# Optimization experiments

Measured on AMD Instinct MI355X. Metric: run time of the kernel, lower is better.

## Reference

```python
import jax, jax.numpy as jnp
import numpy as np
from math import factorial

MAXL = 5
TAUS = [8, 8, 8, 8, 8, 8]
OUT_TAUS = [8, 8, 8, 8, 8, 8]
BM_EPS = 1e-5
BATCH = 1024


def _cg_coeff(l1, l2, l, m1, m2, m):
    # Standard Clebsch-Gordan coefficient <l1 m1 l2 m2 | l m> (Racah formula).
    if m1 + m2 != m:
        return 0.0
    f = factorial
    pre = ((2 * l + 1) * f(l + l1 - l2) * f(l - l1 + l2) * f(l1 + l2 - l) / f(l1 + l2 + l + 1)) ** 0.5
    pre *= (f(l + m) * f(l - m) * f(l1 - m1) * f(l1 + m1) * f(l2 - m2) * f(l2 + m2)) ** 0.5
    s = 0.0
    for k in range(0, l1 + l2 - l + 1):
        ds = [k, l1 + l2 - l - k, l1 - m1 - k, l2 + m2 - k, l - l2 + m1 + k, l - l1 - m2 + k]
        if min(ds) < 0:
            continue
        d = 1.0
        for v in ds:
            d *= f(v)
        s += (-1.0) ** k / d
    return pre * s


def _cg_block(l1, l2, l):
    C = np.zeros((2 * l + 1, 2 * l1 + 1, 2 * l2 + 1), dtype=np.float32)
    for m in range(-l, l + 1):
        for m1 in range(-l1, l1 + 1):
            m2 = m - m1
            if -l2 <= m2 <= l2:
                C[m + l, m1 + l1, m2 + l2] = _cg_coeff(l1, l2, l, m1, m2, m)
    return C


# Triple enumeration order matches cal_middle_taus (l1 outer, l2, then l).
TRIPLES = []
for _l1 in range(MAXL + 1):
    for _l2 in range(_l1 + 1):
        for _l in range(_l1 - _l2, min(_l1 + _l2, MAXL) + 1):
            TRIPLES.append((_l1, _l2, _l))
CG_BLOCKS = [jnp.asarray(_cg_block(*t)) for t in TRIPLES]

MIDDLE_TAUS = np.zeros(MAXL + 1, dtype=np.int64)
for (_l1, _l2, _l) in TRIPLES:
    MIDDLE_TAUS[_l] += TAUS[_l1] * TAUS[_l2]
IN_LEN = int(sum(TAUS[l] * (2 * l + 1) for l in range(MAXL + 1)))    # 288
OUT_LEN = int(sum(OUT_TAUS[l] * (2 * l + 1) for l in range(MAXL + 1)))  # 288
WLEN = int(sum(OUT_TAUS[l] * int(MIDDLE_TAUS[l]) for l in range(MAXL + 1)))  # 35328
STD_LEN = int(MIDDLE_TAUS.sum())  # 4416


def _forward(activations, weights, moving_std):
    B = activations.shape[0]
    act = activations[..., 0] + 1j * activations[..., 1]  # [B, IN_LEN] complex64
    # split into per-degree blocks F[l]: [B, tau_l, 2l+1]
    F = []
    st = 0
    for l in range(MAXL + 1):
        n = TAUS[l] * (2 * l + 1)
        F.append(act[:, st:st + n].reshape(B, TAUS[l], 2 * l + 1))
        st += n
    # CG tensor product: one fragment per (l1,l2,l) triple, grouped by output degree l
    mids = [[] for _ in range(MAXL + 1)]
    for (l1, l2, l), C in zip(TRIPLES, CG_BLOCKS):
        frag = jnp.einsum('mac,bta,bsc->btsm', C.astype(act.dtype), F[l1], F[l2])
        mids[l].append(frag.reshape(B, TAUS[l1] * TAUS[l2], 2 * l + 1))
    # per-fragment batchnorm (divide by running std) + per-degree complex mixing
    outs = []
    so = 0
    wo = 0
    for l in range(MAXL + 1):
        mid = jnp.concatenate(mids[l], axis=1)  # [B, middle_taus[l], 2l+1]
        nt = int(MIDDLE_TAUS[l])
        std = moving_std[so:so + nt]
        so += nt
        mid = mid / (std + BM_EPS)[None, :, None]
        nw = OUT_TAUS[l] * nt
        wl = weights[wo:wo + nw]
        wo += nw
        Wc = (wl[:, 0] + 1j * wl[:, 1]).reshape(OUT_TAUS[l], nt)
        out = jnp.einsum('ot,btm->bom', Wc, mid)  # [B, out_taus[l], 2l+1]
        outs.append(out.reshape(B, OUT_TAUS[l] * (2 * l + 1)))
    oc = jnp.concatenate(outs, axis=1)  # [B, OUT_LEN] complex
    return jnp.stack([oc.real, oc.imag], axis=-1)  # [B, OUT_LEN, 2]


def setup_inputs() -> dict:
    key = jax.random.key(0)
    k1, k2, k3 = jax.random.split(key, 3)
    activations = jax.random.normal(k1, (BATCH, IN_LEN, 2), dtype=jnp.float32)
    weights = 0.05 * jax.random.uniform(k2, (WLEN, 2), dtype=jnp.float32)
    moving_std = 0.1 + 0.9 * jax.random.uniform(k3, (STD_LEN,), dtype=jnp.float32)
    return {"activations": activations, "weights": weights, "moving_std": moving_std}


def reference(activations, weights, moving_std):
    return _forward(activations, weights, moving_std)
```

## Files before the change

### kernel.cpp

```cpp
#include <hip/hip_runtime.h>
#include <hip/hip_bf16.h>
#include <utility>


constexpr int NTRIP = 69;
constexpr int NL    = 6;
constexpr int BATCH = 1024;
constexpr int ROW   = 288;
constexpr int MID_LDS = 2112;

struct Meta {
    int tl1[NTRIP], tl2[NTRIP], tll[NTRIP];
    int tf1[NTRIP], tf2[NTRIP];
    int ttloc[NTRIP];
    int trip_of_l[NL][16];
    int ntrips[NL];
    int mid_tau[NL], std_off[NL], w_off[NL], f_l[NL];
    int nch[NL];
    int ch_start[NL][8], ch_cnt[NL][8];
    int wave_of[NL][16];
};

constexpr Meta build_meta() {
    Meta m{};
    int fl[NL] = {};
    {
        int acc = 0;
        for (int l = 0; l < NL; l++) { fl[l] = acc; m.f_l[l] = acc; acc += 8 * (2 * l + 1); }
    }
    int idx = 0;
    for (int l1 = 0; l1 <= 5; l1++)
        for (int l2 = 0; l2 <= l1; l2++) {
            int lmax = (l1 + l2 < 5) ? (l1 + l2) : 5;
            for (int l = l1 - l2; l <= lmax; l++) {
                m.tl1[idx] = l1; m.tl2[idx] = l2; m.tll[idx] = l;
                m.tf1[idx] = fl[l1]; m.tf2[idx] = fl[l2];
                m.ttloc[idx] = 64 * m.ntrips[l];
                m.trip_of_l[l][m.ntrips[l]] = idx;
                m.ntrips[l]++;
                idx++;
            }
        }
    int so = 0, wo = 0;
    for (int l = 0; l < NL; l++) {
        m.mid_tau[l] = 64 * m.ntrips[l];
        m.std_off[l] = so; so += m.mid_tau[l];
        m.w_off[l]   = wo; wo += 8 * m.mid_tau[l];
    }
    for (int l = 0; l < NL; l++) {
        const int TW = 2 * l + 1;
        const int maxslot = MID_LDS / (64 * TW);
        const int ntl = m.ntrips[l];
        const int nch = (ntl + maxslot - 1) / maxslot;
        m.nch[l] = nch;
        int done = 0;
        for (int c = 0; c < nch; c++) {
            int cnt = (ntl - done + (nch - c) - 1) / (nch - c);
            m.ch_start[l][c] = done; m.ch_cnt[l][c] = cnt; done += cnt;
        }
        for (int c = 0; c < nch; c++) {
            const int s0 = m.ch_start[l][c], cnt = m.ch_cnt[l][c];
            int cost[16] = {}; bool asg[16] = {};
            for (int i = 0; i < cnt; i++) {
                int trip = m.trip_of_l[l][s0 + i];
                int l1 = m.tl1[trip], l2 = m.tl2[trip];
                int tc = 0;
                for (int mi = 0; mi < TW; mi++) {
                    int base = mi - l;
                    int lo = base + l1 - l2; if (lo < 0) lo = 0;
                    int hi = base + l1 + l2; if (hi > 2 * l1) hi = 2 * l1;
                    tc += hi - lo + 1;
                }
                cost[i] = tc * 6 + (2 * l1 + 1 + 2 * l2 + 1) * 2;
            }
            int load[4] = {};
            for (int k = 0; k < cnt; k++) {
                int best = -1, bc = -1;
                for (int i = 0; i < cnt; i++)
                    if (!asg[i] && cost[i] > bc) { bc = cost[i]; best = i; }
                asg[best] = true;
                int wsel = 0;
                for (int w2 = 1; w2 < 4; w2++) if (load[w2] < load[wsel]) wsel = w2;
                m.wave_of[l][s0 + best] = wsel;
                load[wsel] += bc;
            }
        }
    }
    return m;
}

constexpr Meta MT = build_meta();
constexpr int WLEN = 35328;
static_assert(MT.w_off[5] + 8 * MT.mid_tau[5] == WLEN, "wlen");
static_assert(MT.std_off[5] + MT.mid_tau[5] == 4416, "stdlen");
static_assert(MT.nch[0] + MT.nch[1] + MT.nch[2] + MT.nch[5] == 9, "grpA");
static_assert(MT.nch[3] + MT.nch[4] == 9, "grpB");

constexpr double cfact(int n) {
    double r = 1.0;
    for (int i = 2; i <= n; i++) r *= (double)i;
    return r;
}
constexpr double csqrt(double x) {
    double g = x > 1.0 ? x : 1.0;
    for (int i = 0; i < 100; i++) g = 0.5 * (g + x / g);
    return g;
}
constexpr float cg_coeff(int l1, int l2, int l, int m1, int m2, int m) {
    if (m1 + m2 != m) return 0.0f;
    double pre = csqrt((double)(2 * l + 1) * cfact(l + l1 - l2) * cfact(l - l1 + l2) *
                       cfact(l1 + l2 - l) / cfact(l1 + l2 + l + 1));
    pre *= csqrt(cfact(l + m) * cfact(l - m) * cfact(l1 - m1) * cfact(l1 + m1) *
                 cfact(l2 - m2) * cfact(l2 + m2));
    double s = 0.0;
    for (int k = 0; k <= l1 + l2 - l; k++) {
        int d0 = k, d1 = l1 + l2 - l - k, d2 = l1 - m1 - k;
        int d3 = l2 + m2 - k, d4 = l - l2 + m1 + k, d5 = l - l1 - m2 + k;
        if (d0 < 0 || d1 < 0 || d2 < 0 || d3 < 0 || d4 < 0 || d5 < 0) continue;
        double den = cfact(d0) * cfact(d1) * cfact(d2) * cfact(d3) * cfact(d4) * cfact(d5);
        s += ((k & 1) ? -1.0 : 1.0) / den;
    }
    return (float)(pre * s);
}

template <int... Is, class F>
__device__ __forceinline__ void static_for_impl(std::integer_sequence<int, Is...>, F&& f) {
    (f(std::integral_constant<int, Is>{}), ...);
}
template <int N, class F>
__device__ __forceinline__ void static_for(F&& f) {
    static_for_impl(std::make_integer_sequence<int, N>{}, (F&&)f);
}

template <int L>
__device__ __forceinline__ void process_l(int b, int tid,
                                          const float2* __restrict__ F,
                                          float2* __restrict__ mid,
                                          const float2* __restrict__ w,
                                          const float* __restrict__ stdv,
                                          float2* __restrict__ out) {
    constexpr int TW  = 2 * L + 1;
    constexpr int NCH = MT.nch[L];
    constexpr int NT  = MT.mid_tau[L];

    const int wid  = tid >> 6;
    const int lane = tid & 63;
    const int t = lane >> 3, s = lane & 7;

    float2 acc0[TW], acc1[TW];
#pragma unroll
    for (int i = 0; i < TW; i++) { acc0[i] = make_float2(0.f, 0.f); acc1[i] = make_float2(0.f, 0.f); }

    static_for<NCH>([&](auto CHc) {
        constexpr int CH  = decltype(CHc)::value;
        constexpr int S0  = MT.ch_start[L][CH];
        constexpr int CNT = MT.ch_cnt[L][CH];
        constexpr int CT  = CNT * 64;
        static_assert(CT * TW <= MID_LDS, "chunk fits");

        __syncthreads();

        static_for<CNT>([&](auto SIc) {
            constexpr int SI   = S0 + decltype(SIc)::value;
            constexpr int TRIP = MT.trip_of_l[L][SI];
            constexpr int L1   = MT.tl1[TRIP];
            constexpr int L2v  = MT.tl2[TRIP];
            constexpr int N1   = 2 * L1 + 1, N2 = 2 * L2v + 1;
            if (MT.wave_of[L][SI] == wid) {
                const float inv = 1.0f /
                    (stdv[MT.std_off[L] + MT.ttloc[TRIP] + lane] + 1e-5f);
                const float2* F1 = F + MT.tf1[TRIP] + t * N1;
                const float2* F2 = F + MT.tf2[TRIP] + s * N2;
                float2 f1[N1], f2[N2];
#pragma unroll
                for (int i = 0; i < N1; i++) f1[i] = F1[i];
#pragma unroll
                for (int i = 0; i < N2; i++) f2[i] = F2[i];
                const int Tloc = (MT.ttloc[TRIP] - S0 * 64) + lane;
                static_for<TW>([&](auto MIc) {
                    constexpr int MI   = decltype(MIc)::value;
                    constexpr int BASE = MI - L;
                    constexpr int LO_  = BASE + L1 - L2v;
                    constexpr int LO   = LO_ < 0 ? 0 : LO_;
                    constexpr int HI_  = BASE + L1 + L2v;
                    constexpr int HI   = HI_ > 2 * L1 ? 2 * L1 : HI_;
                    float re = 0.f, im = 0.f;
                    static_for<HI - LO + 1>([&](auto Kc) {
                        constexpr int AI = LO + decltype(Kc)::value;
                        constexpr int CI = BASE + L1 + L2v - AI;
                        constexpr float cv = cg_coeff(L1, L2v, L, AI - L1, CI - L2v, BASE);
                        if constexpr (cv != 0.0f) {
                            const float2 a = f1[AI], c2 = f2[CI];
                            re = fmaf(cv, fmaf(-a.y, c2.y, a.x * c2.x), re);
                            im = fmaf(cv, fmaf(a.y, c2.x, a.x * c2.y), im);
                        }
                    });
                    mid[MI * CT + Tloc] = make_float2(re * inv, im * inv);
                });
            }
        });
        __syncthreads();

        {
            const float2* W0 = w + MT.w_off[L] + wid * NT + S0 * 64;
            const float2* W1 = w + MT.w_off[L] + (wid + 4) * NT + S0 * 64;
            for (int T = lane * 2; T < CT; T += 128) {
                const float4 w0 = *reinterpret_cast<const float4*>(W0 + T);
                const float4 w1 = *reinterpret_cast<const float4*>(W1 + T);
#pragma unroll
                for (int mi = 0; mi < TW; mi++) {
                    const float4 mv = *reinterpret_cast<const float4*>(mid + mi * CT + T);
                    acc0[mi].x = fmaf(w0.x, mv.x, fmaf(-w0.y, mv.y,
                                  fmaf(w0.z, mv.z, fmaf(-w0.w, mv.w, acc0[mi].x))));
                    acc0[mi].y = fmaf(w0.x, mv.y, fmaf(w0.y, mv.x,
                                  fmaf(w0.z, mv.w, fmaf(w0.w, mv.z, acc0[mi].y))));
                    acc1[mi].x = fmaf(w1.x, mv.x, fmaf(-w1.y, mv.y,
                                  fmaf(w1.z, mv.z, fmaf(-w1.w, mv.w, acc1[mi].x))));
                    acc1[mi].y = fmaf(w1.x, mv.y, fmaf(w1.y, mv.x,
                                  fmaf(w1.z, mv.w, fmaf(w1.w, mv.z, acc1[mi].y))));
                }
            }
        }
    });

    const bool lo = (lane < 32);
    float2 red[TW];
#pragma unroll
    for (int mi = 0; mi < TW; mi++) {
        float gx = lo ? acc1[mi].x : acc0[mi].x;
        float gy = lo ? acc1[mi].y : acc0[mi].y;
        float rx = (lo ? acc0[mi].x : acc1[mi].x) + __shfl_xor(gx, 32, 64);
        float ry = (lo ? acc0[mi].y : acc1[mi].y) + __shfl_xor(gy, 32, 64);
#pragma unroll
        for (int off = 16; off >= 1; off >>= 1) {
            rx += __shfl_xor(rx, off, 64);
            ry += __shfl_xor(ry, off, 64);
        }
        red[mi] = make_float2(rx, ry);
    }
    if (lane == 0 || lane == 32) {
        const int o = wid + (lo ? 0 : 4);
        float2* orow = out + (size_t)b * ROW + MT.f_l[L] + o * TW;
#pragma unroll
        for (int mi = 0; mi < TW; mi++) orow[mi] = red[mi];
    }
}

__global__ __launch_bounds__(256, 4) void fup_main(const float2* __restrict__ act,
                                                   const float2* __restrict__ w,
                                                   const float* __restrict__ stdv,
                                                   float2* __restrict__ out) {
    __shared__ float2 F[ROW];
    __shared__ __align__(16) float2 mid[MID_LDS];
    const int bid = blockIdx.x;
    const int grp = bid & 1;
    const int b   = bid >> 1;
    const int tid = threadIdx.x;
    const float2* arow = act + (size_t)b * ROW;
    for (int i = tid; i < ROW; i += 256) F[i] = arow[i];
    if (grp == 0) {
        process_l<0>(b, tid, F, mid, w, stdv, out);
        process_l<1>(b, tid, F, mid, w, stdv, out);
        process_l<2>(b, tid, F, mid, w, stdv, out);
        process_l<5>(b, tid, F, mid, w, stdv, out);
    } else {
        process_l<3>(b, tid, F, mid, w, stdv, out);
        process_l<4>(b, tid, F, mid, w, stdv, out);
    }
}

extern "C" void kernel_launch(void* const* d_in, const int* in_sizes, int n_in,
                              void* d_out, int out_size, void* d_ws, size_t ws_size,
                              hipStream_t stream) {
    const float2* act  = (const float2*)d_in[0];
    const float2* wts  = (const float2*)d_in[1];
    const float*  stdv = (const float*)d_in[2];
    float2* out = (float2*)d_out;
    (void)d_ws; (void)ws_size;

    hipLaunchKernelGGL(fup_main, dim3(2 * BATCH), dim3(256), 0, stream,
                       act, wts, stdv, out);
}
```

Before: 123.9 us.

## Use one 16-wave block per batch row with cross-wave LDS reduction

Replaces two 256-thread blocks per batch row (split by degree groups) with a single 1024-thread block per row that processes all six degrees. Triples are balanced across 16 waves, and the weight contraction is split so each wave handles one output channel and half of the middle-tau range. Partial sums go through an LDS buffer that is double-buffered by degree parity, and the final reduction for each degree overlaps the start of the next degree. Chunk metadata and the mid buffer size change to fit larger chunks. Larger blocks add more barrier cost and may lower occupancy in exchange for more parallelism per row.

Measured after the change: 196.0 us. 1.58x slower.

```diff
diff --git a/kernel.cpp b/kernel.cpp
--- a/kernel.cpp
+++ b/kernel.cpp
@@ -7,7 +7,8 @@
 constexpr int NL    = 6;
 constexpr int BATCH = 1024;
 constexpr int ROW   = 288;
-constexpr int MID_LDS = 2112;
+constexpr int MID_LDS = 4224;
+constexpr int NWAVES  = 16;
 
 struct Meta {
     int tl1[NTRIP], tl2[NTRIP], tll[NTRIP];
@@ -17,7 +18,7 @@
     int ntrips[NL];
     int mid_tau[NL], std_off[NL], w_off[NL], f_l[NL];
     int nch[NL];
-    int ch_start[NL][8], ch_cnt[NL][8];
+    int ch_start[NL][2], ch_cnt[NL][2];
     int wave_of[NL][16];
 };
 
@@ -73,14 +74,14 @@
                 }
                 cost[i] = tc * 6 + (2 * l1 + 1 + 2 * l2 + 1) * 2;
             }
-            int load[4] = {};
+            int load[NWAVES] = {};
             for (int k = 0; k < cnt; k++) {
                 int best = -1, bc = -1;
                 for (int i = 0; i < cnt; i++)
                     if (!asg[i] && cost[i] > bc) { bc = cost[i]; best = i; }
                 asg[best] = true;
                 int wsel = 0;
-                for (int w2 = 1; w2 < 4; w2++) if (load[w2] < load[wsel]) wsel = w2;
+                for (int w2 = 1; w2 < NWAVES; w2++) if (load[w2] < load[wsel]) wsel = w2;
                 m.wave_of[l][s0 + best] = wsel;
                 load[wsel] += bc;
             }
@@ -93,8 +94,9 @@
 constexpr int WLEN = 35328;
 static_assert(MT.w_off[5] + 8 * MT.mid_tau[5] == WLEN, "wlen");
 static_assert(MT.std_off[5] + MT.mid_tau[5] == 4416, "stdlen");
-static_assert(MT.nch[0] + MT.nch[1] + MT.nch[2] + MT.nch[5] == 9, "grpA");
-static_assert(MT.nch[3] + MT.nch[4] == 9, "grpB");
+
+constexpr int REDW = 11;
+constexpr int REDBUF = 2 * NWAVES * REDW;
 
 constexpr double cfact(int n) {
     double r = 1.0;
@@ -132,13 +134,35 @@
     static_for_impl(std::make_integer_sequence<int, N>{}, (F&&)f);
 }
 
+template <int P>
+__device__ __forceinline__ void epilogue(int b, int tid,
+                                         const float2* __restrict__ redbuf,
+                                         float2* __restrict__ out) {
+    constexpr int TWp = 2 * P + 1;
+    const int wid = tid >> 6, lane = tid & 63;
+    if (wid == NWAVES - 1) {
+#pragma unroll
+        for (int i0 = 0; i0 < 8 * TWp; i0 += 64) {
+            const int i = i0 + lane;
+            if (i < 8 * TWp) {
+                const int o = i / TWp, m = i % TWp;
+                const float2 a = redbuf[(P & 1) * NWAVES * REDW + o * REDW + m];
+                const float2 c = redbuf[(P & 1) * NWAVES * REDW + (o + 8) * REDW + m];
+                out[(size_t)b * ROW + MT.f_l[P] + o * TWp + m] =
+                    make_float2(a.x + c.x, a.y + c.y);
+            }
+        }
+    }
+}
+
 template <int L>
 __device__ __forceinline__ void process_l(int b, int tid,
                                           const float2* __restrict__ F,
                                           float2* __restrict__ mid,
                                           const float2* __restrict__ w,
                                           const float* __restrict__ stdv,
-                                          float2* __restrict__ out) {
+                                          float2* __restrict__ out,
+                                          float2* __restrict__ redbuf) {
     constexpr int TW  = 2 * L + 1;
     constexpr int NCH = MT.nch[L];
     constexpr int NT  = MT.mid_tau[L];
@@ -147,9 +171,9 @@
     const int lane = tid & 63;
     const int t = lane >> 3, s = lane & 7;
 
-    float2 acc0[TW], acc1[TW];
-#pragma unroll
-    for (int i = 0; i < TW; i++) { acc0[i] = make_float2(0.f, 0.f); acc1[i] = make_float2(0.f, 0.f); }
+    float2 acc[TW];
+#pragma unroll
+    for (int i = 0; i < TW; i++) acc[i] = make_float2(0.f, 0.f);
 
     static_for<NCH>([&](auto CHc) {
         constexpr int CH  = decltype(CHc)::value;
@@ -159,6 +183,9 @@
         static_assert(CT * TW <= MID_LDS, "chunk fits");
 
         __syncthreads();
+
+        if constexpr (CH == 0 && L > 0)
+            epilogue<L - 1>(b, tid, redbuf, out);
 
         static_for<CNT>([&](auto SIc) {
             constexpr int SI   = S0 + decltype(SIc)::value;
@@ -202,71 +229,59 @@
         __syncthreads();
 
         {
-            const float2* W0 = w + MT.w_off[L] + wid * NT + S0 * 64;
-            const float2* W1 = w + MT.w_off[L] + (wid + 4) * NT + S0 * 64;
-            for (int T = lane * 2; T < CT; T += 128) {
+            const int o = wid & 7, half = wid >> 3;
+            const float2* W0 = w + MT.w_off[L] + o * NT + S0 * 64;
+            for (int T = lane * 2 + half * 128; T < CT; T += 256) {
                 const float4 w0 = *reinterpret_cast<const float4*>(W0 + T);
-                const float4 w1 = *reinterpret_cast<const float4*>(W1 + T);
 #pragma unroll
                 for (int mi = 0; mi < TW; mi++) {
                     const float4 mv = *reinterpret_cast<const float4*>(mid + mi * CT + T);
-                    acc0[mi].x = fmaf(w0.x, mv.x, fmaf(-w0.y, mv.y,
-                                  fmaf(w0.z, mv.z, fmaf(-w0.w, mv.w, acc0[mi].x))));
-                    acc0[mi].y = fmaf(w0.x, mv.y, fmaf(w0.y, mv.x,
-                                  fmaf(w0.z, mv.w, fmaf(w0.w, mv.z, acc0[mi].y))));
-                    acc1[mi].x = fmaf(w1.x, mv.x, fmaf(-w1.y, mv.y,
-                                  fmaf(w1.z, mv.z, fmaf(-w1.w, mv.w, acc1[mi].x))));
-                    acc1[mi].y = fmaf(w1.x, mv.y, fmaf(w1.y, mv.x,
-                                  fmaf(w1.z, mv.w, fmaf(w1.w, mv.z, acc1[mi].y))));
+                    acc[mi].x = fmaf(w0.x, mv.x, fmaf(-w0.y, mv.y,
+                                  fmaf(w0.z, mv.z, fmaf(-w0.w, mv.w, acc[mi].x))));
+                    acc[mi].y = fmaf(w0.x, mv.y, fmaf(w0.y, mv.x,
+                                  fmaf(w0.z, mv.w, fmaf(w0.w, mv.z, acc[mi].y))));
                 }
             }
         }
     });
 
-    const bool lo = (lane < 32);
     float2 red[TW];
 #pragma unroll
     for (int mi = 0; mi < TW; mi++) {
-        float gx = lo ? acc1[mi].x : acc0[mi].x;
-        float gy = lo ? acc1[mi].y : acc0[mi].y;
-        float rx = (lo ? acc0[mi].x : acc1[mi].x) + __shfl_xor(gx, 32, 64);
-        float ry = (lo ? acc0[mi].y : acc1[mi].y) + __shfl_xor(gy, 32, 64);
-#pragma unroll
-        for (int off = 16; off >= 1; off >>= 1) {
+        float rx = acc[mi].x, ry = acc[mi].y;
+#pragma unroll
+        for (int off = 32; off >= 1; off >>= 1) {
             rx += __shfl_xor(rx, off, 64);
             ry += __shfl_xor(ry, off, 64);
         }
         red[mi] = make_float2(rx, ry);
     }
-    if (lane == 0 || lane == 32) {
-        const int o = wid + (lo ? 0 : 4);
-        float2* orow = out + (size_t)b * ROW + MT.f_l[L] + o * TW;
-#pragma unroll
-        for (int mi = 0; mi < TW; mi++) orow[mi] = red[mi];
-    }
-}
-
-__global__ __launch_bounds__(256, 4) void fup_main(const float2* __restrict__ act,
-                                                   const float2* __restrict__ w,
-                                                   const float* __restrict__ stdv,
-                                                   float2* __restrict__ out) {
+    if (lane == 0) {
+#pragma unroll
+        for (int mi = 0; mi < TW; mi++)
+            redbuf[(L & 1) * NWAVES * REDW + wid * REDW + mi] = red[mi];
+    }
+}
+
+__global__ __launch_bounds__(1024, 4) void fup_main(const float2* __restrict__ act,
+                                                    const float2* __restrict__ w,
+                                                    const float* __restrict__ stdv,
+                                                    float2* __restrict__ out) {
     __shared__ float2 F[ROW];
     __shared__ __align__(16) float2 mid[MID_LDS];
-    const int bid = blockIdx.x;
-    const int grp = bid & 1;
-    const int b   = bid >> 1;
+    __shared__ float2 redbuf[REDBUF];
+    const int b = blockIdx.x;
     const int tid = threadIdx.x;
     const float2* arow = act + (size_t)b * ROW;
-    for (int i = tid; i < ROW; i += 256) F[i] = arow[i];
-    if (grp == 0) {
-        process_l<0>(b, tid, F, mid, w, stdv, out);
-        process_l<1>(b, tid, F, mid, w, stdv, out);
-        process_l<2>(b, tid, F, mid, w, stdv, out);
-        process_l<5>(b, tid, F, mid, w, stdv, out);
-    } else {
-        process_l<3>(b, tid, F, mid, w, stdv, out);
-        process_l<4>(b, tid, F, mid, w, stdv, out);
-    }
+    for (int i = tid; i < ROW; i += 1024) F[i] = arow[i];
+    process_l<0>(b, tid, F, mid, w, stdv, out, redbuf);
+    process_l<1>(b, tid, F, mid, w, stdv, out, redbuf);
+    process_l<2>(b, tid, F, mid, w, stdv, out, redbuf);
+    process_l<3>(b, tid, F, mid, w, stdv, out, redbuf);
+    process_l<4>(b, tid, F, mid, w, stdv, out, redbuf);
+    process_l<5>(b, tid, F, mid, w, stdv, out, redbuf);
+    __syncthreads();
+    epilogue<5>(b, tid, redbuf, out);
 }
 
 extern "C" void kernel_launch(void* const* d_in, const int* in_sizes, int n_in,
@@ -278,6 +293,6 @@
     float2* out = (float2*)d_out;
     (void)d_ws; (void)ws_size;
 
-    hipLaunchKernelGGL(fup_main, dim3(2 * BATCH), dim3(256), 0, stream,
+    hipLaunchKernelGGL(fup_main, dim3(BATCH), dim3(1024), 0, stream,
                        act, wts, stdv, out);
 }
```

## Process two batch rows per 512-thread block with larger mid chunks

Applied to the files above, without the earlier changes.

Work is now split across the block differently. Before, each batch row was handled by two 256-thread blocks that divided the output degrees between them. Now one 512-thread block handles two batch rows, and each 256-thread half computes all six degrees for its own row. The mid staging buffer in LDS is doubled so fewer chunks are needed per degree, which cuts the number of chunk passes and synchronisations. In exchange, LDS per block rises to roughly 72 KB, which limits how many blocks fit per CU. Block-wide barriers also now couple the two independent halves.

New measurement: 122.6 us. Within noise of the previous version (-1.1%).

```diff
diff --git a/kernel.cpp b/kernel.cpp
--- a/kernel.cpp
+++ b/kernel.cpp
@@ -7,7 +7,7 @@
 constexpr int NL    = 6;
 constexpr int BATCH = 1024;
 constexpr int ROW   = 288;
-constexpr int MID_LDS = 2112;
+constexpr int MID_LDS = 4224;
 
 struct Meta {
     int tl1[NTRIP], tl2[NTRIP], tll[NTRIP];
@@ -17,7 +17,7 @@
     int ntrips[NL];
     int mid_tau[NL], std_off[NL], w_off[NL], f_l[NL];
     int nch[NL];
-    int ch_start[NL][8], ch_cnt[NL][8];
+    int ch_start[NL][2], ch_cnt[NL][2];
     int wave_of[NL][16];
 };
 
@@ -93,8 +93,6 @@
 constexpr int WLEN = 35328;
 static_assert(MT.w_off[5] + 8 * MT.mid_tau[5] == WLEN, "wlen");
 static_assert(MT.std_off[5] + MT.mid_tau[5] == 4416, "stdlen");
-static_assert(MT.nch[0] + MT.nch[1] + MT.nch[2] + MT.nch[5] == 9, "grpA");
-static_assert(MT.nch[3] + MT.nch[4] == 9, "grpB");
 
 constexpr double cfact(int n) {
     double r = 1.0;
@@ -246,27 +244,25 @@
     }
 }
 
-__global__ __launch_bounds__(256, 4) void fup_main(const float2* __restrict__ act,
+__global__ __launch_bounds__(512, 4) void fup_main(const float2* __restrict__ act,
                                                    const float2* __restrict__ w,
                                                    const float* __restrict__ stdv,
                                                    float2* __restrict__ out) {
-    __shared__ float2 F[ROW];
-    __shared__ __align__(16) float2 mid[MID_LDS];
-    const int bid = blockIdx.x;
-    const int grp = bid & 1;
-    const int b   = bid >> 1;
-    const int tid = threadIdx.x;
+    __shared__ float2 F[2][ROW];
+    __shared__ __align__(16) float2 mid[2][MID_LDS];
+    const int half = threadIdx.x >> 8;
+    const int tidg = threadIdx.x & 255;
+    const int b    = (blockIdx.x << 1) | half;
+    float2* midh = mid[half];
+    float2* Fh   = F[half];
     const float2* arow = act + (size_t)b * ROW;
-    for (int i = tid; i < ROW; i += 256) F[i] = arow[i];
-    if (grp == 0) {
-        process_l<0>(b, tid, F, mid, w, stdv, out);
-        process_l<1>(b, tid, F, mid, w, stdv, out);
-        process_l<2>(b, tid, F, mid, w, stdv, out);
-        process_l<5>(b, tid, F, mid, w, stdv, out);
-    } else {
-        process_l<3>(b, tid, F, mid, w, stdv, out);
-        process_l<4>(b, tid, F, mid, w, stdv, out);
-    }
+    for (int i = tidg; i < ROW; i += 256) Fh[i] = arow[i];
+    process_l<0>(b, tidg, Fh, midh, w, stdv, out);
+    process_l<1>(b, tidg, Fh, midh, w, stdv, out);
+    process_l<2>(b, tidg, Fh, midh, w, stdv, out);
+    process_l<3>(b, tidg, Fh, midh, w, stdv, out);
+    process_l<4>(b, tidg, Fh, midh, w, stdv, out);
+    process_l<5>(b, tidg, Fh, midh, w, stdv, out);
 }
 
 extern "C" void kernel_launch(void* const* d_in, const int* in_sizes, int n_in,
@@ -278,6 +274,6 @@
     float2* out = (float2*)d_out;
     (void)d_ws; (void)ws_size;
 
-    hipLaunchKernelGGL(fup_main, dim3(2 * BATCH), dim3(256), 0, stream,
+    hipLaunchKernelGGL(fup_main, dim3(BATCH / 2), dim3(512), 0, stream,
                        act, wts, stdv, out);
 }
```
